# Performance work log

Measured on AMD Instinct MI355X. Metric: run time of the kernel, lower is better.

Reference implementation:

```python
import jax, jax.numpy as jnp
import numpy as np

N = 50_000      # node_num
E = 1_600_000   # n_edges (avg degree 32)
D = 256         # input feature dim
H = 128         # GCN / hidden units
FC = 1024       # fc0 units
C = 16          # num_classes


def _tn(key, shape, std=0.1):
    # truncated normal in [-2, 2] std, matching tf.random.truncated_normal(stddev=0.1)
    return jax.random.truncated_normal(key, -2.0, 2.0, shape, jnp.float32) * std


def setup_inputs() -> dict:
    key = jax.random.key(0)
    ks = jax.random.split(key, 16)
    return {
        "x": jax.random.normal(ks[0], (N, D), jnp.float32),
        "edge_index": jax.random.randint(ks[1], (2, E), 0, N, jnp.int32),
        # GCN layer params (tfg GCN: kernel + bias)
        "gcn0_W": _tn(ks[2], (D, H)), "gcn0_b": jnp.zeros((H,), jnp.float32),
        "gcn1_W": _tn(ks[3], (H, H)), "gcn1_b": jnp.zeros((H,), jnp.float32),
        "gcn2_W": _tn(ks[4], (H, H)), "gcn2_b": jnp.zeros((H,), jnp.float32),
        # extra dense block between gcn10 and gcn11
        "w1": _tn(ks[5], (H, H)), "b1": _tn(ks[6], (N, H)),
        # fc head
        "fc0_W": _tn(ks[7], (H, FC)), "fc0_b": jnp.zeros((FC,), jnp.float32),
        "fc1_W": _tn(ks[8], (FC, C)), "fc1_b": jnp.zeros((C,), jnp.float32),
    }


def reference(x, edge_index, gcn0_W, gcn0_b, gcn1_W, gcn1_b, gcn2_W, gcn2_b,
              w1, b1, fc0_W, fc0_b, fc1_W, fc1_b):
    n = x.shape[0]
    src, dst = edge_index[0], edge_index[1]
    loops = jnp.arange(n, dtype=src.dtype)
    # GCN renormalization trick: A_hat = A + I, w_ij = deg_i^-1/2 * deg_j^-1/2
    src_f = jnp.concatenate([src, loops])   # [E+N]
    dst_f = jnp.concatenate([dst, loops])
    deg = jax.ops.segment_sum(jnp.ones(src_f.shape[0], jnp.float32), src_f, num_segments=n)
    norm = jnp.where(deg > 0, deg, 1.0) ** -0.5
    ew = norm[src_f] * norm[dst_f]          # [E+N]

    def gcn(h, W, b):
        h = h @ W                                                      # [N,H]
        agg = jax.ops.segment_sum(h[src_f] * ew[:, None], dst_f, num_segments=n)
        return agg + b

    h1 = jax.nn.relu(gcn(x, gcn0_W, gcn0_b))       # gcn10, relu
    h11 = jax.nn.relu(h1 @ w1 + b1)                # dense with per-node bias
    h2 = gcn(h11, gcn1_W, gcn1_b)                  # gcn11, no activation
    h2 = jax.nn.relu(gcn(h2, gcn2_W, gcn2_b))      # gcn12, relu
    h = h1 + h2
    h = jax.nn.relu(h @ fc0_W + fc0_b)             # fc0
    return h @ fc1_W + fc1_b                       # fc1 logits [N,C]
```

## Files before the change

kernel.cpp:

```cpp
#include <hip/hip_runtime.h>
#include <hip/hip_bf16.h>
#include <hip/hip_fp16.h>
#include <cstddef>
#include <cstdint>

#define NNODES 50000
#define NEDGES 1600000
#define DIM 256
#define HID 128
#define FCU 1024
#define NCLS 16

#define NBKT 256
#define BW 196
#define NBLK_A 64
#define EPB (NEDGES / NBLK_A)
#define CAPB 8192

#define DCHUNK 12800
#define DSLICE 64
#define DEPB (NEDGES / DSLICE)

typedef short s16x8 __attribute__((ext_vector_type(8)));
typedef _Float16 f16x8 __attribute__((ext_vector_type(8)));
typedef float f32x4 __attribute__((ext_vector_type(4)));
#define MFMA16 __builtin_amdgcn_mfma_f32_16x16x32_bf16
#define MFMAH  __builtin_amdgcn_mfma_f32_16x16x32_f16

typedef unsigned short u16;
typedef unsigned int u32;

__device__ inline u16 f2bf(float f) {
    u32 u = __float_as_uint(f);
    return (u16)((u + 0x7FFF + ((u >> 16) & 1)) >> 16);
}
__device__ inline float bf2f(u16 h) { return __uint_as_float(((u32)h) << 16); }
__device__ inline void split2(float v, u16& h, u16& l) {
    h = f2bf(v);
    l = f2bf(v - bf2f(h));
}


__global__ __launch_bounds__(256) void histDeg(const int* __restrict__ ei, int* __restrict__ degS) {
    __shared__ int h[DCHUNK];
    int chunk = blockIdx.x >> 6;
    int slice = blockIdx.x & (DSLICE - 1);
    int t = threadIdx.x;
    int base0 = chunk * DCHUNK;
    for (int i = t; i < DCHUNK; i += 256) h[i] = 0;
    __syncthreads();
    int base = slice * DEPB;
    for (int e = base + t; e < base + DEPB; e += 256) {
        int s = ei[e] - base0;
        if ((unsigned)s < (unsigned)DCHUNK) atomicAdd(&h[s], 1);
    }
    __syncthreads();
    int lim = NNODES - base0; if (lim > DCHUNK) lim = DCHUNK;
    for (int i = t; i < lim; i += 256) {
        int v = h[i];
        if (v) atomicAdd(&degS[base0 + i], v);
    }
}

__global__ void norm_kernel(const int* __restrict__ degS, float* __restrict__ nrm) {
    int i = blockIdx.x * blockDim.x + threadIdx.x;
    if (i < NNODES) nrm[i] = rsqrtf((float)(degS[i] + 1));
}

__global__ __launch_bounds__(1024) void histA(const int* __restrict__ ei, int* __restrict__ hist) {
    __shared__ int h[NBKT];
    int blk = blockIdx.x, t = threadIdx.x;
    if (t < NBKT) h[t] = 0;
    __syncthreads();
    int base = blk * EPB;
    for (int e = base + t; e < base + EPB; e += 1024) {
        int dst = ei[NEDGES + e];
        atomicAdd(&h[dst / BW], 1);
    }
    __syncthreads();
    if (t < NBKT) hist[t * NBLK_A + blk] = h[t];
}

__global__ __launch_bounds__(1024) void scanh_a(int* __restrict__ hist, int* __restrict__ bsum) {
    __shared__ int s[1024];
    int b = blockIdx.x, t = threadIdx.x, i = b * 1024 + t;
    int v = hist[i];
    s[t] = v;
    __syncthreads();
    for (int off = 1; off < 1024; off <<= 1) {
        int x = (t >= off) ? s[t - off] : 0;
        __syncthreads();
        s[t] += x;
        __syncthreads();
    }
    hist[i] = s[t] - v;
    if (t == 1023) bsum[b] = s[1023];
}
__global__ void scanh_b(int* __restrict__ bsum) {
    if (threadIdx.x == 0 && blockIdx.x == 0) {
        int a = 0;
        for (int j = 0; j < 16; ++j) { int t = bsum[j]; bsum[j] = a; a += t; }
    }
}
__global__ __launch_bounds__(1024) void scanh_c(int* __restrict__ hist, const int* __restrict__ bsum) {
    int i = blockIdx.x * 1024 + threadIdx.x;
    hist[i] += bsum[blockIdx.x];
}

__global__ __launch_bounds__(1024) void bucket_fill(const int* __restrict__ ei,
                                                    const int* __restrict__ hist,
                                                    u32* __restrict__ packed) {
    __shared__ int cur[NBKT];
    int blk = blockIdx.x, t = threadIdx.x;
    if (t < NBKT) cur[t] = hist[t * NBLK_A + blk];
    __syncthreads();
    int base = blk * EPB;
    for (int e = base + t; e < base + EPB; e += 1024) {
        int src = ei[e], dst = ei[NEDGES + e];
        int p = atomicAdd(&cur[dst / BW], 1);
        packed[p] = ((u32)dst << 16) | (u32)src;
    }
}

__global__ __launch_bounds__(256) void bucket_csr(const u32* __restrict__ packed,
                                                  const int* __restrict__ hist,
                                                  int* __restrict__ rowptr, u16* __restrict__ csr) {
    __shared__ u32 st[CAPB];
    __shared__ u16 so[CAPB];
    __shared__ int cnt[256], excl[256];
    int b = blockIdx.x, t = threadIdx.x;
    int ebase = hist[b * NBLK_A];
    int eend  = (b < NBKT - 1) ? hist[(b + 1) * NBLK_A] : NEDGES;
    int nE = eend - ebase;
    if (nE > CAPB) nE = CAPB;
    cnt[t] = 0;
    __syncthreads();
    for (int i = t; i < nE; i += 256) {
        u32 p = packed[ebase + i];
        st[i] = p;
        atomicAdd(&cnt[(int)(p >> 16) - b * BW], 1);
    }
    __syncthreads();
    int v = cnt[t];
    excl[t] = v;
    __syncthreads();
    for (int off = 1; off < 256; off <<= 1) {
        int x = (t >= off) ? excl[t - off] : 0;
        __syncthreads();
        excl[t] += x;
        __syncthreads();
    }
    int ex = excl[t] - v;
    int node = b * BW + t;
    if (t < BW && node < NNODES) rowptr[node] = ebase + ex;
    if (b == NBKT - 1 && t == 0) rowptr[NNODES] = NEDGES;
    cnt[t] = ex;
    __syncthreads();
    for (int i = t; i < nE; i += 256) {
        u32 p = st[i];
        int pos = atomicAdd(&cnt[(int)(p >> 16) - b * BW], 1);
        so[pos] = (u16)(p & 0xFFFF);
    }
    __syncthreads();
    for (int i = t; i < nE; i += 256) csr[ebase + i] = so[i];
}


__global__ __launch_bounds__(256) void conv_x(const float* __restrict__ x,
                                              u16* __restrict__ xh, u16* __restrict__ xl) {
    int i = blockIdx.x * blockDim.x + threadIdx.x;
    const float4 v = *reinterpret_cast<const float4*>(x + (size_t)i * 4);
    u16 h0, l0, h1, l1, h2, l2, h3, l3;
    split2(v.x, h0, l0); split2(v.y, h1, l1); split2(v.z, h2, l2); split2(v.w, h3, l3);
    ushort4 hv = make_ushort4(h0, h1, h2, h3), lv = make_ushort4(l0, l1, l2, l3);
    *reinterpret_cast<ushort4*>(xh + (size_t)i * 4) = hv;
    *reinterpret_cast<ushort4*>(xl + (size_t)i * 4) = lv;
}

__global__ __launch_bounds__(256) void conv_wT(const float* __restrict__ W, int K, int N,
                                               u16* __restrict__ outH, u16* __restrict__ outL) {
    int o = blockIdx.x * blockDim.x + threadIdx.x;
    if (o < K * N) {
        int n = o / K, k = o - n * K;
        u16 h, l;
        split2(W[(size_t)k * N + n], h, l);
        outH[o] = h; outL[o] = l;
    }
}

__global__ __launch_bounds__(256) void conv_weights(
    const float* __restrict__ fc0W, u16* __restrict__ F0Th,
    const float* __restrict__ w1,    u16* __restrict__ w1Th,
    const float* __restrict__ gcn1W, u16* __restrict__ W1Th,
    const float* __restrict__ gcn2W, u16* __restrict__ W2Th,
    const float* __restrict__ fc1W,  __half* __restrict__ W1f)
{
    int b = blockIdx.x, t = threadIdx.x;
    if (b < 512) {
        int o = b * 256 + t;
        int n = o >> 7, k = o & 127;
        F0Th[o] = f2bf(fc0W[(size_t)k * FCU + n]);
    } else if (b < 576) {
        int o = (b - 512) * 256 + t;
        int n = o >> 7, k = o & 127;
        w1Th[o] = f2bf(w1[(size_t)k * HID + n]);
    } else if (b < 640) {
        int o = (b - 576) * 256 + t;
        int n = o >> 7, k = o & 127;
        W1Th[o] = f2bf(gcn1W[(size_t)k * HID + n]);
    } else if (b < 704) {
        int o = (b - 640) * 256 + t;
        int n = o >> 7, k = o & 127;
        W2Th[o] = f2bf(gcn2W[(size_t)k * HID + n]);
    } else {
        int o = (b - 704) * 256 + t;
        int n = o >> 10, k = o & 1023;
        W1f[o] = __float2half(fc1W[(size_t)k * NCLS + n]);
    }
}


template<int VAR, int WLO>
__global__ __launch_bounds__(256) void agg_fast(
    const __half* __restrict__ g, const float* __restrict__ nrm,
    const int* __restrict__ rowptr, const u16* __restrict__ csr,
    const float* __restrict__ bias,
    const u16* __restrict__ h1H, const u16* __restrict__ h1L,
    u16* __restrict__ outH, u16* __restrict__ outL)
{
    int w = threadIdx.x >> 6, lane = threadIdx.x & 63;
    int i = blockIdx.x * 4 + w;
    if (i >= NNODES) return;
    const __half2* gp = reinterpret_cast<const __half2*>(g);
    size_t lrow = (size_t)i * 64 + lane;
    float2 acc = __half22float2(gp[lrow]);
    int e0 = rowptr[i], e1 = rowptr[i + 1];
    int e = e0;
    for (; e + 8 <= e1; e += 8) {
        int s[8];
#pragma unroll
        for (int q = 0; q < 8; ++q) s[q] = csr[e + q];
        __half2 v[8];
#pragma unroll
        for (int q = 0; q < 8; ++q) v[q] = gp[(size_t)s[q] * 64 + lane];
#pragma unroll
        for (int q = 0; q < 8; ++q) {
            float2 f = __half22float2(v[q]);
            acc.x += f.x; acc.y += f.y;
        }
    }
    for (; e < e1; ++e) {
        int s = csr[e];
        float2 f = __half22float2(gp[(size_t)s * 64 + lane]);
        acc.x += f.x; acc.y += f.y;
    }
    float ni = nrm[i];
    const float2 b = *reinterpret_cast<const float2*>(bias + lane * 2);
    float v0 = fmaf(ni, acc.x, b.x);
    float v1 = fmaf(ni, acc.y, b.y);
    if (VAR != 1) { v0 = fmaxf(v0, 0.f); v1 = fmaxf(v1, 0.f); }
    if (VAR == 2) {
        ushort2 rh = *reinterpret_cast<const ushort2*>(h1H + (size_t)i * HID + lane * 2);
        ushort2 rl = *reinterpret_cast<const ushort2*>(h1L + (size_t)i * HID + lane * 2);
        v0 += bf2f(rh.x) + bf2f(rl.x);
        v1 += bf2f(rh.y) + bf2f(rl.y);
    }
    if (WLO) {
        u16 h0, l0, h1v, l1v;
        split2(v0, h0, l0);
        split2(v1, h1v, l1v);
        *reinterpret_cast<ushort2*>(outH + (size_t)i * HID + lane * 2) = make_ushort2(h0, h1v);
        *reinterpret_cast<ushort2*>(outL + (size_t)i * HID + lane * 2) = make_ushort2(l0, l1v);
    } else {
        *reinterpret_cast<ushort2*>(outH + (size_t)i * HID + lane * 2) = make_ushort2(f2bf(v0), f2bf(v1));
    }
}


template<int K>
__global__ __launch_bounds__(256) void gemm_split(
    const u16* __restrict__ Ah, const u16* __restrict__ Al,
    const u16* __restrict__ BTh, const u16* __restrict__ BTl,
    const float* __restrict__ nrmv, __half* __restrict__ outG, int M)
{
    const int PK = 40;
    __shared__ __align__(16) u16 AsH[64 * PK], AsL[64 * PK];
    __shared__ __align__(16) u16 BsH[128 * PK], BsL[128 * PK];
    int tid = threadIdx.x, lane = tid & 63, w = tid >> 6;
    int wr = w >> 1, wc = w & 1;
    int l15 = lane & 15, l4 = lane >> 4;
    int blockRow = blockIdx.x * 64;
    f32x4 acc[2][4] = {};

    for (int kk = 0; kk < K; kk += 32) {
        {
            int row = tid >> 2, kc = (tid & 3) * 8;
            int gr = blockRow + row; if (gr >= M) gr = M - 1;
            *(s16x8*)&AsH[row * PK + kc] = *(const s16x8*)&Ah[(size_t)gr * K + kk + kc];
            *(s16x8*)&AsL[row * PK + kc] = *(const s16x8*)&Al[(size_t)gr * K + kk + kc];
        }
#pragma unroll
        for (int i2 = 0; i2 < 2; ++i2) {
            int idx = tid + i2 * 256;
            int n = idx >> 2, kc = (idx & 3) * 8;
            *(s16x8*)&BsH[n * PK + kc] = *(const s16x8*)&BTh[(size_t)n * K + kk + kc];
            *(s16x8*)&BsL[n * PK + kc] = *(const s16x8*)&BTl[(size_t)n * K + kk + kc];
        }
        __syncthreads();
        s16x8 ah[2], al[2], bh[4], bl[4];
#pragma unroll
        for (int mi = 0; mi < 2; ++mi) {
            ah[mi] = *(const s16x8*)&AsH[(wr * 32 + mi * 16 + l15) * PK + 8 * l4];
            al[mi] = *(const s16x8*)&AsL[(wr * 32 + mi * 16 + l15) * PK + 8 * l4];
        }
#pragma unroll
        for (int ni = 0; ni < 4; ++ni) {
            bh[ni] = *(const s16x8*)&BsH[(wc * 64 + ni * 16 + l15) * PK + 8 * l4];
            bl[ni] = *(const s16x8*)&BsL[(wc * 64 + ni * 16 + l15) * PK + 8 * l4];
        }
#pragma unroll
        for (int mi = 0; mi < 2; ++mi)
#pragma unroll
            for (int ni = 0; ni < 4; ++ni) {
                acc[mi][ni] = MFMA16(ah[mi], bh[ni], acc[mi][ni], 0, 0, 0);
                acc[mi][ni] = MFMA16(ah[mi], bl[ni], acc[mi][ni], 0, 0, 0);
                acc[mi][ni] = MFMA16(al[mi], bh[ni], acc[mi][ni], 0, 0, 0);
            }
        __syncthreads();
    }
#pragma unroll
    for (int mi = 0; mi < 2; ++mi)
#pragma unroll
        for (int ni = 0; ni < 4; ++ni) {
            int c = wc * 64 + ni * 16 + l15;
#pragma unroll
            for (int j = 0; j < 4; ++j) {
                int r = blockRow + wr * 32 + mi * 16 + l4 * 4 + j;
                if (r < M) outG[(size_t)r * 128 + c] = __float2half(nrmv[r] * acc[mi][ni][j]);
            }
        }
}


template<int MODE>
__global__ __launch_bounds__(256) void gemm_sp1(
    const u16* __restrict__ Ah, const u16* __restrict__ BTh,
    const float* __restrict__ pnb, const float* __restrict__ nrmv,
    __half* __restrict__ outG, u16* __restrict__ outH, int M)
{
    const int PK = 40;
    __shared__ __align__(16) u16 AsH[128 * PK];
    __shared__ __align__(16) u16 BsH[128 * PK];
    int tid = threadIdx.x, lane = tid & 63, w = tid >> 6;
    int wr = w >> 1, wc = w & 1;
    int l15 = lane & 15, l4 = lane >> 4;
    int blockRow = blockIdx.x * 128;
    f32x4 acc[4][4] = {};

    for (int kk = 0; kk < HID; kk += 32) {
#pragma unroll
        for (int i2 = 0; i2 < 2; ++i2) {
            int idx = tid + i2 * 256;
            int row = idx >> 2, kc = (idx & 3) * 8;
            int gr = blockRow + row; if (gr >= M) gr = M - 1;
            *(s16x8*)&AsH[row * PK + kc] = *(const s16x8*)&Ah[(size_t)gr * HID + kk + kc];
            *(s16x8*)&BsH[row * PK + kc] = *(const s16x8*)&BTh[(size_t)row * HID + kk + kc];
        }
        __syncthreads();
        s16x8 ah[4], bh[4];
#pragma unroll
        for (int mi = 0; mi < 4; ++mi)
            ah[mi] = *(const s16x8*)&AsH[(wr * 64 + mi * 16 + l15) * PK + 8 * l4];
#pragma unroll
        for (int ni = 0; ni < 4; ++ni)
            bh[ni] = *(const s16x8*)&BsH[(wc * 64 + ni * 16 + l15) * PK + 8 * l4];
#pragma unroll
        for (int mi = 0; mi < 4; ++mi)
#pragma unroll
            for (int ni = 0; ni < 4; ++ni)
                acc[mi][ni] = MFMA16(ah[mi], bh[ni], acc[mi][ni], 0, 0, 0);
        __syncthreads();
    }
#pragma unroll
    for (int mi = 0; mi < 4; ++mi)
#pragma unroll
        for (int ni = 0; ni < 4; ++ni) {
            int c = wc * 64 + ni * 16 + l15;
#pragma unroll
            for (int j = 0; j < 4; ++j) {
                int r = blockRow + wr * 64 + mi * 16 + l4 * 4 + j;
                if (r < M) {
                    if (MODE == 0) {
                        outG[(size_t)r * 128 + c] = __float2half(nrmv[r] * acc[mi][ni][j]);
                    } else {
                        float v = fmaxf(acc[mi][ni][j] + pnb[(size_t)r * 128 + c], 0.f);
                        outH[(size_t)r * 128 + c] = f2bf(v);
                    }
                }
            }
        }
}


__global__ __launch_bounds__(256) void fc_kernel(
    const u16* __restrict__ Ahi,
    const u16* __restrict__ BTh,
    const float* __restrict__ fc0b,
    const __half* __restrict__ W1f,
    const float* __restrict__ fc1b,
    float* __restrict__ out, int M)
{
    __shared__ __align__(16) u16 vs[32 * 128];
    __shared__ __align__(16) u16 W1s[16 * 128];
    int tid = threadIdx.x, lane = tid & 63, w = tid >> 6;
    int l15 = lane & 15, l4 = lane >> 4;
    int blockRow = blockIdx.x * 32;

    s16x8 ahr[2][4];
#pragma unroll
    for (int mi = 0; mi < 2; ++mi) {
        int r = blockRow + mi * 16 + l15; if (r >= M) r = M - 1;
#pragma unroll
        for (int ks = 0; ks < 4; ++ks)
            ahr[mi][ks] = *(const s16x8*)&Ahi[(size_t)r * HID + ks * 32 + 8 * l4];
    }

    f32x4 acc2 = {0.f, 0.f, 0.f, 0.f};
    s16x8 bcur[2][4];
#pragma unroll
    for (int ni = 0; ni < 2; ++ni)
#pragma unroll
        for (int ks = 0; ks < 4; ++ks)
            bcur[ni][ks] = *(const s16x8*)&BTh[(size_t)(w * 32 + ni * 16 + l15) * HID + ks * 32 + 8 * l4];

#pragma unroll
    for (int cc = 0; cc < FCU / 128; ++cc) {
        int co = cc * 128;
        s16x8 bnxt[2][4];
        if (cc + 1 < FCU / 128) {
#pragma unroll
            for (int ni = 0; ni < 2; ++ni)
#pragma unroll
                for (int ks = 0; ks < 4; ++ks)
                    bnxt[ni][ks] = *(const s16x8*)&BTh[(size_t)(co + 128 + w * 32 + ni * 16 + l15) * HID + ks * 32 + 8 * l4];
        }

        f32x4 acc[2][2] = {};
#pragma unroll
        for (int ks = 0; ks < 4; ++ks)
#pragma unroll
            for (int mi = 0; mi < 2; ++mi)
#pragma unroll
                for (int ni = 0; ni < 2; ++ni)
                    acc[mi][ni] = MFMA16(ahr[mi][ks], bcur[ni][ks], acc[mi][ni], 0, 0, 0);

        {
            int cls = tid >> 4, kc = (tid & 15) * 8;
            s16x8 t = *(const s16x8*)&W1f[(size_t)cls * FCU + co + kc];
            *(s16x8*)&W1s[cls * 128 + (kc ^ ((cls & 7) << 3))] = t;
        }
#pragma unroll
        for (int mi = 0; mi < 2; ++mi)
#pragma unroll
            for (int ni = 0; ni < 2; ++ni) {
                int unit = w * 32 + ni * 16 + l15;
                float b0v = fc0b[co + unit];
#pragma unroll
                for (int j = 0; j < 4; ++j) {
                    int rl = mi * 16 + l4 * 4 + j;
                    float v = fmaxf(acc[mi][ni][j] + b0v, 0.f);
                    vs[rl * 128 + (unit ^ ((rl & 7) << 3))] = __half_as_ushort(__float2half(v));
                }
            }
        __syncthreads();

        if (w < 2) {
#pragma unroll
            for (int ks = 0; ks < 4; ++ks) {
                int row = w * 16 + l15;
                int colk = ks * 32 + 8 * l4;
                f16x8 a2 = *(const f16x8*)&vs[row * 128 + (colk ^ ((row & 7) << 3))];
                f16x8 b2 = *(const f16x8*)&W1s[l15 * 128 + (colk ^ ((l15 & 7) << 3))];
                acc2 = MFMAH(a2, b2, acc2, 0, 0, 0);
            }
        }
        __syncthreads();

        if (cc + 1 < FCU / 128) {
#pragma unroll
            for (int ni = 0; ni < 2; ++ni)
#pragma unroll
                for (int ks = 0; ks < 4; ++ks)
                    bcur[ni][ks] = bnxt[ni][ks];
        }
    }

    if (w < 2) {
#pragma unroll
        for (int j = 0; j < 4; ++j) {
            int gr = blockRow + w * 16 + l4 * 4 + j;
            if (gr < M) out[(size_t)gr * NCLS + l15] = acc2[j] + fc1b[l15];
        }
    }
}


extern "C" void kernel_launch(void* const* d_in, const int* in_sizes, int n_in,
                              void* d_out, int out_size, void* d_ws, size_t ws_size,
                              hipStream_t stream)
{
    const float* x     = (const float*)d_in[0];
    const int*   ei    = (const int*)d_in[1];
    const float* gcn0W = (const float*)d_in[2];
    const float* gcn0b = (const float*)d_in[3];
    const float* gcn1W = (const float*)d_in[4];
    const float* gcn1b = (const float*)d_in[5];
    const float* gcn2W = (const float*)d_in[6];
    const float* gcn2b = (const float*)d_in[7];
    const float* w1    = (const float*)d_in[8];
    const float* b1    = (const float*)d_in[9];
    const float* fc0W  = (const float*)d_in[10];
    const float* fc0b  = (const float*)d_in[11];
    const float* fc1W  = (const float*)d_in[12];
    const float* fc1b  = (const float*)d_in[13];
    float* out = (float*)d_out;

    char* ws = (char*)d_ws;
    size_t off = 0;
    auto alloc = [&](size_t bytes) -> void* {
        void* p = ws + off;
        off = (off + bytes + 255) & ~(size_t)255;
        return p;
    };
    int* degS   = (int*)alloc((size_t)NNODES * 4);
    int* rowptr = (int*)alloc((size_t)(NNODES + 1) * 4);
    int* hist   = (int*)alloc((size_t)NBKT * NBLK_A * 4);
    int* bsum   = (int*)alloc(64 * 4);
    u32* packed = (u32*)alloc((size_t)NEDGES * 4);
    u16* csr    = (u16*)alloc((size_t)NEDGES * 2);
    float* nrm  = (float*)alloc((size_t)NNODES * 4);
    u16* W0Th = (u16*)alloc((size_t)DIM * HID * 2);  u16* W0Tl = (u16*)alloc((size_t)DIM * HID * 2);
    u16* w1Th = (u16*)alloc((size_t)HID * HID * 2);
    u16* W1Th = (u16*)alloc((size_t)HID * HID * 2);
    u16* W2Th = (u16*)alloc((size_t)HID * HID * 2);
    u16* F0Th = (u16*)alloc((size_t)HID * FCU * 2);
    __half* W1f = (__half*)alloc((size_t)FCU * NCLS * 2);
    __half* bufG = (__half*)alloc((size_t)NNODES * HID * 2);
    u16* R1 = (u16*)alloc((size_t)2 * NNODES * DIM * 2);
    u16* xh = R1, *xl = R1 + (size_t)NNODES * DIM;
    u16* h1H = R1,                            *h1L = R1 + (size_t)NNODES * HID;
    u16* B3H = R1 + (size_t)2 * NNODES * HID;

    const int M = NNODES;
    hipMemsetAsync(degS, 0, (size_t)NNODES * 4, stream);

    histDeg<<<4 * DSLICE, 256, 0, stream>>>(ei, degS);
    norm_kernel<<<(NNODES + 255) / 256, 256, 0, stream>>>(degS, nrm);
    histA<<<NBLK_A, 1024, 0, stream>>>(ei, hist);
    scanh_a<<<16, 1024, 0, stream>>>(hist, bsum);
    scanh_b<<<1, 64, 0, stream>>>(bsum);
    scanh_c<<<16, 1024, 0, stream>>>(hist, bsum);
    bucket_fill<<<NBLK_A, 1024, 0, stream>>>(ei, hist, packed);
    bucket_csr<<<NBKT, 256, 0, stream>>>(packed, hist, rowptr, csr);

    conv_x<<<(NNODES * DIM / 4 + 255) / 256, 256, 0, stream>>>(x, xh, xl);
    conv_wT<<<(DIM * HID + 255) / 256, 256, 0, stream>>>(gcn0W, DIM, HID, W0Th, W0Tl);
    conv_weights<<<768, 256, 0, stream>>>(fc0W, F0Th, w1, w1Th, gcn1W, W1Th, gcn2W, W2Th, fc1W, W1f);

    const int GB = (M + 63) / 64;
    const int GB128 = (M + 127) / 128;
    const int GB32 = (M + 31) / 32;
    const int AB = (NNODES + 3) / 4;
    gemm_split<DIM><<<GB, 256, 0, stream>>>(xh, xl, W0Th, W0Tl, nrm, bufG, M);
    agg_fast<0, 1><<<AB, 256, 0, stream>>>(bufG, nrm, rowptr, csr, gcn0b, nullptr, nullptr, h1H, h1L);
    gemm_sp1<2><<<GB128, 256, 0, stream>>>(h1H, w1Th, b1, nullptr, nullptr, B3H, M);
    gemm_sp1<0><<<GB128, 256, 0, stream>>>(B3H, W1Th, nullptr, nrm, bufG, nullptr, M);
    agg_fast<1, 0><<<AB, 256, 0, stream>>>(bufG, nrm, rowptr, csr, gcn1b, nullptr, nullptr, B3H, nullptr);
    gemm_sp1<0><<<GB128, 256, 0, stream>>>(B3H, W2Th, nullptr, nrm, bufG, nullptr, M);
    agg_fast<2, 0><<<AB, 256, 0, stream>>>(bufG, nrm, rowptr, csr, gcn2b, h1H, h1L, B3H, nullptr);
    fc_kernel<<<GB32, 256, 0, stream>>>(B3H, F0Th, fc0b, W1f, fc1b, out, M);
}
```

Measured before the change: 427.1 us.

## Fuse final aggregation into FC head and unify GEMM kernels with 64-row tiles

Folds the third GCN aggregation (with bias, relu and the h1 residual) into the FC kernel. Each block aggregates its 32 rows into a swizzled LDS tile and feeds them straight into the fc0/fc1 MFMA path, so the intermediate h buffer is never written to or read back from global memory. The single-precision 128-wide GEMMs now run through a templated gemm_split with 64-row tiles instead of the 128-row gemm_sp1. That doubles the block count but halves per-block reuse. The fused kernel puts the latency-bound gather in the same blocks as the MFMA work, and each wave handles 8 rows serially, which may reduce latency hiding in the gather.

Result: slower. 470.7 us (+10.2%).

```diff
diff --git a/kernel.cpp b/kernel.cpp
--- a/kernel.cpp
+++ b/kernel.cpp
@@ -225,7 +225,6 @@
     const __half* __restrict__ g, const float* __restrict__ nrm,
     const int* __restrict__ rowptr, const u16* __restrict__ csr,
     const float* __restrict__ bias,
-    const u16* __restrict__ h1H, const u16* __restrict__ h1L,
     u16* __restrict__ outH, u16* __restrict__ outL)
 {
     int w = threadIdx.x >> 6, lane = threadIdx.x & 63;
@@ -259,12 +258,6 @@
     float v0 = fmaf(ni, acc.x, b.x);
     float v1 = fmaf(ni, acc.y, b.y);
     if (VAR != 1) { v0 = fmaxf(v0, 0.f); v1 = fmaxf(v1, 0.f); }
-    if (VAR == 2) {
-        ushort2 rh = *reinterpret_cast<const ushort2*>(h1H + (size_t)i * HID + lane * 2);
-        ushort2 rl = *reinterpret_cast<const ushort2*>(h1L + (size_t)i * HID + lane * 2);
-        v0 += bf2f(rh.x) + bf2f(rl.x);
-        v1 += bf2f(rh.y) + bf2f(rl.y);
-    }
     if (WLO) {
         u16 h0, l0, h1v, l1v;
         split2(v0, h0, l0);
@@ -277,15 +270,18 @@
 }
 
 
-template<int K>
+template<int K, int MODE, int PL>
 __global__ __launch_bounds__(256) void gemm_split(
     const u16* __restrict__ Ah, const u16* __restrict__ Al,
     const u16* __restrict__ BTh, const u16* __restrict__ BTl,
-    const float* __restrict__ nrmv, __half* __restrict__ outG, int M)
+    const float* __restrict__ pnb, const float* __restrict__ nrmv,
+    __half* __restrict__ outG, u16* __restrict__ outH, int M)
 {
     const int PK = 40;
-    __shared__ __align__(16) u16 AsH[64 * PK], AsL[64 * PK];
-    __shared__ __align__(16) u16 BsH[128 * PK], BsL[128 * PK];
+    __shared__ __align__(16) u16 AsH[64 * PK];
+    __shared__ __align__(16) u16 BsH[128 * PK];
+    __shared__ __align__(16) u16 AsL[PL == 3 ? 64 * PK : 1];
+    __shared__ __align__(16) u16 BsL[PL == 3 ? 128 * PK : 1];
     int tid = threadIdx.x, lane = tid & 63, w = tid >> 6;
     int wr = w >> 1, wc = w & 1;
     int l15 = lane & 15, l4 = lane >> 4;
@@ -297,34 +293,38 @@
             int row = tid >> 2, kc = (tid & 3) * 8;
             int gr = blockRow + row; if (gr >= M) gr = M - 1;
             *(s16x8*)&AsH[row * PK + kc] = *(const s16x8*)&Ah[(size_t)gr * K + kk + kc];
-            *(s16x8*)&AsL[row * PK + kc] = *(const s16x8*)&Al[(size_t)gr * K + kk + kc];
+            if (PL == 3)
+                *(s16x8*)&AsL[row * PK + kc] = *(const s16x8*)&Al[(size_t)gr * K + kk + kc];
         }
 #pragma unroll
         for (int i2 = 0; i2 < 2; ++i2) {
             int idx = tid + i2 * 256;
             int n = idx >> 2, kc = (idx & 3) * 8;
             *(s16x8*)&BsH[n * PK + kc] = *(const s16x8*)&BTh[(size_t)n * K + kk + kc];
-            *(s16x8*)&BsL[n * PK + kc] = *(const s16x8*)&BTl[(size_t)n * K + kk + kc];
+            if (PL == 3)
+                *(s16x8*)&BsL[n * PK + kc] = *(const s16x8*)&BTl[(size_t)n * K + kk + kc];
         }
         __syncthreads();
         s16x8 ah[2], al[2], bh[4], bl[4];
 #pragma unroll
         for (int mi = 0; mi < 2; ++mi) {
             ah[mi] = *(const s16x8*)&AsH[(wr * 32 + mi * 16 + l15) * PK + 8 * l4];
-            al[mi] = *(const s16x8*)&AsL[(wr * 32 + mi * 16 + l15) * PK + 8 * l4];
+            if (PL == 3) al[mi] = *(const s16x8*)&AsL[(wr * 32 + mi * 16 + l15) * PK + 8 * l4];
         }
 #pragma unroll
         for (int ni = 0; ni < 4; ++ni) {
             bh[ni] = *(const s16x8*)&BsH[(wc * 64 + ni * 16 + l15) * PK + 8 * l4];
-            bl[ni] = *(const s16x8*)&BsL[(wc * 64 + ni * 16 + l15) * PK + 8 * l4];
+            if (PL == 3) bl[ni] = *(const s16x8*)&BsL[(wc * 64 + ni * 16 + l15) * PK + 8 * l4];
         }
 #pragma unroll
         for (int mi = 0; mi < 2; ++mi)
 #pragma unroll
             for (int ni = 0; ni < 4; ++ni) {
                 acc[mi][ni] = MFMA16(ah[mi], bh[ni], acc[mi][ni], 0, 0, 0);
-                acc[mi][ni] = MFMA16(ah[mi], bl[ni], acc[mi][ni], 0, 0, 0);
-                acc[mi][ni] = MFMA16(al[mi], bh[ni], acc[mi][ni], 0, 0, 0);
+                if (PL == 3) {
+                    acc[mi][ni] = MFMA16(ah[mi], bl[ni], acc[mi][ni], 0, 0, 0);
+                    acc[mi][ni] = MFMA16(al[mi], bh[ni], acc[mi][ni], 0, 0, 0);
+                }
             }
         __syncthreads();
     }
@@ -336,59 +336,6 @@
 #pragma unroll
             for (int j = 0; j < 4; ++j) {
                 int r = blockRow + wr * 32 + mi * 16 + l4 * 4 + j;
-                if (r < M) outG[(size_t)r * 128 + c] = __float2half(nrmv[r] * acc[mi][ni][j]);
-            }
-        }
-}
-
-
-template<int MODE>
-__global__ __launch_bounds__(256) void gemm_sp1(
-    const u16* __restrict__ Ah, const u16* __restrict__ BTh,
-    const float* __restrict__ pnb, const float* __restrict__ nrmv,
-    __half* __restrict__ outG, u16* __restrict__ outH, int M)
-{
-    const int PK = 40;
-    __shared__ __align__(16) u16 AsH[128 * PK];
-    __shared__ __align__(16) u16 BsH[128 * PK];
-    int tid = threadIdx.x, lane = tid & 63, w = tid >> 6;
-    int wr = w >> 1, wc = w & 1;
-    int l15 = lane & 15, l4 = lane >> 4;
-    int blockRow = blockIdx.x * 128;
-    f32x4 acc[4][4] = {};
-
-    for (int kk = 0; kk < HID; kk += 32) {
-#pragma unroll
-        for (int i2 = 0; i2 < 2; ++i2) {
-            int idx = tid + i2 * 256;
-            int row = idx >> 2, kc = (idx & 3) * 8;
-            int gr = blockRow + row; if (gr >= M) gr = M - 1;
-            *(s16x8*)&AsH[row * PK + kc] = *(const s16x8*)&Ah[(size_t)gr * HID + kk + kc];
-            *(s16x8*)&BsH[row * PK + kc] = *(const s16x8*)&BTh[(size_t)row * HID + kk + kc];
-        }
-        __syncthreads();
-        s16x8 ah[4], bh[4];
-#pragma unroll
-        for (int mi = 0; mi < 4; ++mi)
-            ah[mi] = *(const s16x8*)&AsH[(wr * 64 + mi * 16 + l15) * PK + 8 * l4];
-#pragma unroll
-        for (int ni = 0; ni < 4; ++ni)
-            bh[ni] = *(const s16x8*)&BsH[(wc * 64 + ni * 16 + l15) * PK + 8 * l4];
-#pragma unroll
-        for (int mi = 0; mi < 4; ++mi)
-#pragma unroll
-            for (int ni = 0; ni < 4; ++ni)
-                acc[mi][ni] = MFMA16(ah[mi], bh[ni], acc[mi][ni], 0, 0, 0);
-        __syncthreads();
-    }
-#pragma unroll
-    for (int mi = 0; mi < 4; ++mi)
-#pragma unroll
-        for (int ni = 0; ni < 4; ++ni) {
-            int c = wc * 64 + ni * 16 + l15;
-#pragma unroll
-            for (int j = 0; j < 4; ++j) {
-                int r = blockRow + wr * 64 + mi * 16 + l4 * 4 + j;
                 if (r < M) {
                     if (MODE == 0) {
                         outG[(size_t)r * 128 + c] = __float2half(nrmv[r] * acc[mi][ni][j]);
@@ -402,30 +349,24 @@
 }
 
 
-__global__ __launch_bounds__(256) void fc_kernel(
-    const u16* __restrict__ Ahi,
+__global__ __launch_bounds__(256) void agg_fc(
+    const __half* __restrict__ g, const float* __restrict__ nrm,
+    const int* __restrict__ rowptr, const u16* __restrict__ csr,
+    const float* __restrict__ bias,
+    const u16* __restrict__ h1H, const u16* __restrict__ h1L,
     const u16* __restrict__ BTh,
     const float* __restrict__ fc0b,
     const __half* __restrict__ W1f,
     const float* __restrict__ fc1b,
     float* __restrict__ out, int M)
 {
+    __shared__ __align__(16) u16 hA[32 * 128];
     __shared__ __align__(16) u16 vs[32 * 128];
     __shared__ __align__(16) u16 W1s[16 * 128];
     int tid = threadIdx.x, lane = tid & 63, w = tid >> 6;
     int l15 = lane & 15, l4 = lane >> 4;
     int blockRow = blockIdx.x * 32;
 
-    s16x8 ahr[2][4];
-#pragma unroll
-    for (int mi = 0; mi < 2; ++mi) {
-        int r = blockRow + mi * 16 + l15; if (r >= M) r = M - 1;
-#pragma unroll
-        for (int ks = 0; ks < 4; ++ks)
-            ahr[mi][ks] = *(const s16x8*)&Ahi[(size_t)r * HID + ks * 32 + 8 * l4];
-    }
-
-    f32x4 acc2 = {0.f, 0.f, 0.f, 0.f};
     s16x8 bcur[2][4];
 #pragma unroll
     for (int ni = 0; ni < 2; ++ni)
@@ -433,6 +374,60 @@
         for (int ks = 0; ks < 4; ++ks)
             bcur[ni][ks] = *(const s16x8*)&BTh[(size_t)(w * 32 + ni * 16 + l15) * HID + ks * 32 + 8 * l4];
 
+    const __half2* gp = reinterpret_cast<const __half2*>(g);
+    const float2 bb = *reinterpret_cast<const float2*>(bias + lane * 2);
+    int colc = lane >> 2;
+    int colr = (lane * 2) & 7;
+#pragma unroll 1
+    for (int k = 0; k < 8; ++k) {
+        int row = w * 8 + k;
+        int i = blockRow + row;
+        float v0 = 0.f, v1 = 0.f;
+        if (i < M) {
+            float2 acc = __half22float2(gp[(size_t)i * 64 + lane]);
+            int e0 = rowptr[i], e1 = rowptr[i + 1];
+            int e = e0;
+            for (; e + 8 <= e1; e += 8) {
+                int s[8];
+#pragma unroll
+                for (int q = 0; q < 8; ++q) s[q] = csr[e + q];
+                __half2 vv[8];
+#pragma unroll
+                for (int q = 0; q < 8; ++q) vv[q] = gp[(size_t)s[q] * 64 + lane];
+#pragma unroll
+                for (int q = 0; q < 8; ++q) {
+                    float2 f = __half22float2(vv[q]);
+                    acc.x += f.x; acc.y += f.y;
+                }
+            }
+            for (; e < e1; ++e) {
+                float2 f = __half22float2(gp[(size_t)csr[e] * 64 + lane]);
+                acc.x += f.x; acc.y += f.y;
+            }
+            float ni_ = nrm[i];
+            v0 = fmaxf(fmaf(ni_, acc.x, bb.x), 0.f);
+            v1 = fmaxf(fmaf(ni_, acc.y, bb.y), 0.f);
+            ushort2 rh = *reinterpret_cast<const ushort2*>(h1H + (size_t)i * HID + lane * 2);
+            ushort2 rl = *reinterpret_cast<const ushort2*>(h1L + (size_t)i * HID + lane * 2);
+            v0 += bf2f(rh.x) + bf2f(rl.x);
+            v1 += bf2f(rh.y) + bf2f(rl.y);
+        }
+        int cs = colc ^ (row & 7);
+        *reinterpret_cast<ushort2*>(&hA[row * 128 + (cs << 3) + colr]) =
+            make_ushort2(f2bf(v0), f2bf(v1));
+    }
+    __syncthreads();
+
+    s16x8 ahr[2][4];
+#pragma unroll
+    for (int mi = 0; mi < 2; ++mi) {
+        int row = mi * 16 + l15;
+#pragma unroll
+        for (int ks = 0; ks < 4; ++ks)
+            ahr[mi][ks] = *(const s16x8*)&hA[row * 128 + (((ks * 4 + l4) ^ (row & 7)) << 3)];
+    }
+
+    f32x4 acc2 = {0.f, 0.f, 0.f, 0.f};
 #pragma unroll
     for (int cc = 0; cc < FCU / 128; ++cc) {
         int co = cc * 128;
@@ -568,15 +563,14 @@
     conv_weights<<<768, 256, 0, stream>>>(fc0W, F0Th, w1, w1Th, gcn1W, W1Th, gcn2W, W2Th, fc1W, W1f);
 
     const int GB = (M + 63) / 64;
-    const int GB128 = (M + 127) / 128;
     const int GB32 = (M + 31) / 32;
     const int AB = (NNODES + 3) / 4;
-    gemm_split<DIM><<<GB, 256, 0, stream>>>(xh, xl, W0Th, W0Tl, nrm, bufG, M);
-    agg_fast<0, 1><<<AB, 256, 0, stream>>>(bufG, nrm, rowptr, csr, gcn0b, nullptr, nullptr, h1H, h1L);
-    gemm_sp1<2><<<GB128, 256, 0, stream>>>(h1H, w1Th, b1, nullptr, nullptr, B3H, M);
-    gemm_sp1<0><<<GB128, 256, 0, stream>>>(B3H, W1Th, nullptr, nrm, bufG, nullptr, M);
-    agg_fast<1, 0><<<AB, 256, 0, stream>>>(bufG, nrm, rowptr, csr, gcn1b, nullptr, nullptr, B3H, nullptr);
-    gemm_sp1<0><<<GB128, 256, 0, stream>>>(B3H, W2Th, nullptr, nrm, bufG, nullptr, M);
-    agg_fast<2, 0><<<AB, 256, 0, stream>>>(bufG, nrm, rowptr, csr, gcn2b, h1H, h1L, B3H, nullptr);
-    fc_kernel<<<GB32, 256, 0, stream>>>(B3H, F0Th, fc0b, W1f, fc1b, out, M);
-}
+    gemm_split<DIM, 0, 3><<<GB, 256, 0, stream>>>(xh, xl, W0Th, W0Tl, nullptr, nrm, bufG, nullptr, M);
+    agg_fast<0, 1><<<AB, 256, 0, stream>>>(bufG, nrm, rowptr, csr, gcn0b, h1H, h1L);
+    gemm_split<HID, 2, 1><<<GB, 256, 0, stream>>>(h1H, nullptr, w1Th, nullptr, b1, nullptr, nullptr, B3H, M);
+    gemm_split<HID, 0, 1><<<GB, 256, 0, stream>>>(B3H, nullptr, W1Th, nullptr, nullptr, nrm, bufG, nullptr, M);
+    agg_fast<1, 0><<<AB, 256, 0, stream>>>(bufG, nrm, rowptr, csr, gcn1b, B3H, nullptr);
+    gemm_split<HID, 0, 1><<<GB, 256, 0, stream>>>(B3H, nullptr, W2Th, nullptr, nullptr, nrm, bufG, nullptr, M);
+    agg_fc<<<GB32, 256, 0, stream>>>(bufG, nrm, rowptr, csr, gcn2b, h1H, h1L,
+                                     F0Th, fc0b, W1f, fc1b, out, M);
+}
```
